# Performance work log

Measured on AMD Instinct MI355X. Metric: run time of the kernel, lower is better.

The kernel has to match this reference:

```python
import jax, jax.numpy as jnp
import numpy as np

KERNELS = (7, 9, 11)   # kernel_sizes, dilation=1 each
HEADS_PER = 2          # num_head // len(kernel_sizes)
HEAD_DIM = 32          # dim // num_head
DIM = 192


def _win_idx(L, K):
    # NATTEN non-causal window start: centered, clamped to stay in-bounds.
    starts = jnp.clip(jnp.arange(L) - K // 2, 0, L - K)
    return starts[:, None] + jnp.arange(K)[None, :]  # [L, K]


def _na2d(q, k, v, K):
    # q,k,v: [B, h, H, W, D]; q pre-scaled. Neighborhood attention, kernel KxK.
    B, h, H, W, D = q.shape
    ih = _win_idx(H, K)  # [H, K]
    iw = _win_idx(W, K)  # [W, K]
    kr = k[:, :, ih]     # [B, h, H, Kh, W, D]  rows gathered once
    # loop over the Kw kernel taps (small fixed structural loop)
    attn = jnp.stack(
        [jnp.einsum('bnijd,bnikjd->bnijk', q, kr[:, :, :, :, iw[:, kw], :])
         for kw in range(K)], axis=-1)                 # [B,h,H,W,Kh,Kw]
    attn = jax.nn.softmax(attn.reshape(B, h, H, W, K * K), axis=-1)
    attn = attn.reshape(B, h, H, W, K, K)
    vr = v[:, :, ih]     # [B, h, H, Kh, W, D]
    y = jnp.zeros_like(q)
    for kw in range(K):
        y = y + jnp.einsum('bnijk,bnikjd->bnijd',
                           attn[..., kw], vr[:, :, :, :, iw[:, kw], :])
    return y             # [B, h, H, W, D]


def _forward(x, w_qkv, b_qkv, w_proj, b_proj):
    B, H, W, C = x.shape
    qkv = x @ w_qkv + b_qkv                      # [B,H,W,3*DIM]
    scale = HEAD_DIM ** -0.5
    outs = []
    off = 0
    for K in KERNELS:
        ch = 3 * HEADS_PER * HEAD_DIM            # 192 per scale
        xi = qkv[..., off:off + ch]
        off += ch
        r = xi.reshape(B, H, W, 3, HEADS_PER, HEAD_DIM)
        q = jnp.transpose(r[:, :, :, 0], (0, 3, 1, 2, 4)) * scale
        k = jnp.transpose(r[:, :, :, 1], (0, 3, 1, 2, 4))
        v = jnp.transpose(r[:, :, :, 2], (0, 3, 1, 2, 4))
        y = _na2d(q, k, v, K)                    # [B,h,H,W,D]
        outs.append(jnp.transpose(y, (0, 2, 3, 1, 4)).reshape(B, H, W, HEADS_PER * HEAD_DIM))
    out = jnp.concatenate(outs, axis=-1)         # [B,H,W,DIM]
    return out @ w_proj + b_proj


def setup_inputs() -> dict:
    key = jax.random.key(0)
    ks = jax.random.split(key, 4)
    x = jax.random.normal(ks[0], (4, 96, 96, DIM), jnp.float32)
    w_qkv = jax.random.normal(ks[1], (DIM, 3 * DIM), jnp.float32) * 0.02
    b_qkv = jnp.zeros((3 * DIM,), jnp.float32)
    w_proj = jax.random.normal(ks[2], (DIM, DIM), jnp.float32) * 0.02
    b_proj = jnp.zeros((DIM,), jnp.float32)
    return {'x': x, 'w_qkv': w_qkv, 'b_qkv': b_qkv, 'w_proj': w_proj, 'b_proj': b_proj}


def reference(x, w_qkv, b_qkv, w_proj, b_proj):
    return _forward(x, w_qkv, b_qkv, w_proj, b_proj)
```

## Files before the change

### kernel.cpp

```cpp
#include <hip/hip_runtime.h>
#include <cstddef>

constexpr int B_ = 4, H_ = 96, W_ = 96, C_ = 192, QKVC = 576;
constexpr int NPIX = B_ * H_ * W_;
constexpr float SCALE = 0.17677669529663689f;

typedef __attribute__((ext_vector_type(8))) short bf16x8;
typedef __attribute__((ext_vector_type(4))) float f32x4;
typedef unsigned short ushort_t;

__device__ __forceinline__ unsigned short f2bf(float f) {
    unsigned int u = __builtin_bit_cast(unsigned int, f);
    u += 0x7fffu + ((u >> 16) & 1u);
    return (unsigned short)(u >> 16);
}
__device__ __forceinline__ float bf2f(unsigned short h) {
    unsigned int u = ((unsigned int)h) << 16;
    return __builtin_bit_cast(float, u);
}
__device__ __forceinline__ unsigned int pack2(unsigned short a, unsigned short b) {
    return (unsigned int)a | ((unsigned int)b << 16);
}

__global__ __launch_bounds__(256) void convert_x_kernel(
    const float* __restrict__ x, ushort_t* __restrict__ xh, int n4)
{
    int i = blockIdx.x * 256 + threadIdx.x;
    if (i >= n4) return;
    float4 v = ((const float4*)x)[i];
    uint2 p;
    p.x = pack2(f2bf(v.x), f2bf(v.y));
    p.y = pack2(f2bf(v.z), f2bf(v.w));
    ((uint2*)xh)[i] = p;
}

__global__ __launch_bounds__(256) void convert_w_kernel(
    const float* __restrict__ w_qkv, const float* __restrict__ w_proj,
    ushort_t* __restrict__ wqt, ushort_t* __restrict__ wpt_h,
    ushort_t* __restrict__ wpt_l)
{
    int idx = blockIdx.x * 256 + threadIdx.x;
    if (idx < 576 * 192) {
        int n = idx / 192, k = idx - n * 192;
        wqt[idx] = f2bf(w_qkv[(size_t)k * 576 + n]);
    } else {
        int i2 = idx - 576 * 192;
        if (i2 < 192 * 192) {
            int n = i2 / 192, k = i2 - n * 192;
            float v = w_proj[(size_t)k * 192 + n];
            unsigned short h = f2bf(v);
            wpt_h[i2] = h;
            wpt_l[i2] = f2bf(v - bf2f(h));
        }
    }
}

template<bool BSPLIT, bool OUTBF, bool VT>
__global__ __launch_bounds__(256) void gemm_mfma2_kernel(
    const ushort_t* __restrict__ A,
    const ushort_t* __restrict__ Bt_h, const ushort_t* __restrict__ Bt_l,
    const float* __restrict__ bias, void* __restrict__ Cout,
    ushort_t* __restrict__ vTout, int M, int N, int K)
{
    constexpr int NPB = BSPLIT ? 2 : 1;
    __shared__ __align__(16) ushort_t As[8 * 64 * 8];
    __shared__ __align__(16) ushort_t Bs[NPB][8 * 192 * 8];

    const int tid = threadIdx.x;
    const int lane = tid & 63;
    const int w = tid >> 6;
    const int wm = (w & 1) * 32;
    const int wn = (w >> 1) * 96;
    const int fm = lane & 15;
    const int fq = lane >> 4;

    const int ntiles = N / 192;
    const int m0 = (blockIdx.x / ntiles) * 64;
    const int n0 = (blockIdx.x % ntiles) * 192;

    f32x4 acc[2][6];
    #pragma unroll
    for (int mi = 0; mi < 2; ++mi)
        #pragma unroll
        for (int ni = 0; ni < 6; ++ni)
            acc[mi][ni] = (f32x4){0.f, 0.f, 0.f, 0.f};

    for (int k0 = 0; k0 < K; k0 += 64) {
        __syncthreads();
        #pragma unroll
        for (int it = 0; it < 2; ++it) {
            int idx = it * 256 + tid;
            int m = idx >> 3, kc = idx & 7;
            uint4 v = *(const uint4*)(A + (size_t)(m0 + m) * K + k0 + kc * 8);
            *(uint4*)(&As[0] + (kc * 64 + (m ^ kc)) * 8) = v;
        }
        #pragma unroll
        for (int it = 0; it < 6; ++it) {
            int idx = it * 256 + tid;
            int n = idx >> 3, kc = idx & 7;
            int phys = kc * 192 + (n ^ kc);
            *(uint4*)(&Bs[0][0] + phys * 8) =
                *(const uint4*)(Bt_h + (size_t)(n0 + n) * K + k0 + kc * 8);
            if constexpr (BSPLIT)
                *(uint4*)(&Bs[NPB - 1][0] + phys * 8) =
                    *(const uint4*)(Bt_l + (size_t)(n0 + n) * K + k0 + kc * 8);
        }
        __syncthreads();

        #pragma unroll
        for (int kt2 = 0; kt2 < 2; ++kt2) {
            const int kc = kt2 * 4 + fq;
            bf16x8 ah[2], bh[6];
            #pragma unroll
            for (int mi = 0; mi < 2; ++mi)
                ah[mi] = *(const bf16x8*)(&As[0] + (kc * 64 + ((wm + mi * 16 + fm) ^ kc)) * 8);
            #pragma unroll
            for (int ni = 0; ni < 6; ++ni)
                bh[ni] = *(const bf16x8*)(&Bs[0][0] + (kc * 192 + ((wn + ni * 16 + fm) ^ kc)) * 8);
            #pragma unroll
            for (int mi = 0; mi < 2; ++mi)
                #pragma unroll
                for (int ni = 0; ni < 6; ++ni)
                    acc[mi][ni] = __builtin_amdgcn_mfma_f32_16x16x32_bf16(
                        ah[mi], bh[ni], acc[mi][ni], 0, 0, 0);
            if constexpr (BSPLIT) {
                bf16x8 bl[6];
                #pragma unroll
                for (int ni = 0; ni < 6; ++ni)
                    bl[ni] = *(const bf16x8*)(&Bs[NPB - 1][0] + (kc * 192 + ((wn + ni * 16 + fm) ^ kc)) * 8);
                #pragma unroll
                for (int mi = 0; mi < 2; ++mi)
                    #pragma unroll
                    for (int ni = 0; ni < 6; ++ni)
                        acc[mi][ni] = __builtin_amdgcn_mfma_f32_16x16x32_bf16(
                            ah[mi], bl[ni], acc[mi][ni], 0, 0, 0);
            }
        }
    }

    #pragma unroll
    for (int ni = 0; ni < 6; ++ni) {
        const int lcol = wn + ni * 16 + fm;
        const int col = n0 + lcol;
        const float bv = bias[col];
        const int vl = lcol - 128;
        #pragma unroll
        for (int mi = 0; mi < 2; ++mi) {
            const int rbase = m0 + wm + mi * 16 + fq * 4;
            #pragma unroll
            for (int r = 0; r < 4; ++r) {
                float val = acc[mi][ni][r] + bv;
                if constexpr (OUTBF)
                    ((ushort_t*)Cout)[(size_t)(rbase + r) * N + col] = f2bf(val);
                else
                    ((float*)Cout)[(size_t)(rbase + r) * N + col] = val;
                if constexpr (VT) {
                    if (vl >= 0) {
                        int pix = rbase + r;
                        int bb = pix / 9216;
                        int rem = pix - bb * 9216;
                        int ii = rem / 96;
                        int jj = rem - ii * 96;
                        int hh = vl >> 5, dd = vl & 31;
                        vTout[((size_t)((bb * 96 + ii) * 6) + (n0 / 192) * 2 + hh) * 3072
                              + dd * 96 + jj] = f2bf(val);
                    }
                }
            }
        }
    }
}

__global__ __launch_bounds__(384, 5) void na2d_kernel(
    const ushort_t* __restrict__ qkv, const ushort_t* __restrict__ vT,
    ushort_t* __restrict__ attn)
{
    __shared__ ushort_t Kb[2][96 * 40];
    __shared__ ushort_t Vtb[2][32 * 104];
    __shared__ ushort_t Pb[6][16 * 40];

    int idx = blockIdx.x;
    const int g = idx % 3; idx /= 3;
    const int h = idx & 1; idx >>= 1;
    const int i = idx % 96;
    const int b = idx / 96;

    const int K = 7 + 2 * g, cc = K >> 1;
    int si = i - cc; if (si < 0) si = 0; if (si > H_ - K) si = H_ - K;

    const int tid = threadIdx.x;
    const int w = tid >> 6, lane = tid & 63;
    const int fm = lane & 15, fq = lane >> 4;
    const int pixbase = w * 16;

    int cb = (pixbase - cc) & ~7;
    if (cb < 0) cb = 0; if (cb > 64) cb = 64;
    const int col0 = cb + fm, col1 = cb + 16 + fm;

    int sj[4];
    #pragma unroll
    for (int r = 0; r < 4; ++r) {
        int jj = pixbase + fq * 4 + r - cc;
        if (jj < 0) jj = 0; if (jj > W_ - K) jj = W_ - K;
        sj[r] = jj;
    }

    const size_t rowstride = (size_t)W_ * QKVC;
    const bf16x8 qfrag = *(const bf16x8*)(
        qkv + (size_t)(b * H_ + i) * rowstride + (size_t)(pixbase + fm) * QKVC
        + g * 192 + h * 32 + fq * 8);

    const int scol = tid >> 2, sch = tid & 3;
    const size_t kgoff = (size_t)scol * QKVC + g * 192 + 64 + h * 32 + sch * 8;
    const int klds = scol * 40 + ((sch ^ (scol & 3)) << 3);
    const int vd = tid / 12, vc8 = tid - vd * 12;
    const int vlds = vd * 104 + vc8 * 8;
    const size_t vslice = ((size_t)((b * H_ + si) * 6) + g * 2 + h) * 3072;

    f32x4 y0 = {0.f, 0.f, 0.f, 0.f}, y1 = {0.f, 0.f, 0.f, 0.f};
    float lacc[4] = {0.f, 0.f, 0.f, 0.f};

    uint4 kv = *(const uint4*)(qkv + (size_t)(b * H_ + si) * rowstride + kgoff);
    uint4 vv = *(const uint4*)(vT + vslice + (size_t)tid * 8);

    for (int t = 0; t < K; ++t) {
        *(uint4*)&Kb[t & 1][klds] = kv;
        *(uint4*)&Vtb[t & 1][vlds] = vv;
        if (t + 1 < K) {
            kv = *(const uint4*)(qkv + (size_t)(b * H_ + si + t + 1) * rowstride + kgoff);
            vv = *(const uint4*)(vT + vslice + (size_t)(t + 1) * 18432 + (size_t)tid * 8);
        }
        __syncthreads();

        bf16x8 kf0 = *(const bf16x8*)&Kb[t & 1][col0 * 40 + ((fq ^ (col0 & 3)) << 3)];
        bf16x8 kf1 = *(const bf16x8*)&Kb[t & 1][col1 * 40 + ((fq ^ (col1 & 3)) << 3)];
        f32x4 s0 = __builtin_amdgcn_mfma_f32_16x16x32_bf16(
            qfrag, kf0, (f32x4){0.f, 0.f, 0.f, 0.f}, 0, 0, 0);
        f32x4 s1 = __builtin_amdgcn_mfma_f32_16x16x32_bf16(
            qfrag, kf1, (f32x4){0.f, 0.f, 0.f, 0.f}, 0, 0, 0);

        #pragma unroll
        for (int r = 0; r < 4; ++r) {
            float e0 = __expf(s0[r] * SCALE);
            float e1 = __expf(s1[r] * SCALE);
            e0 = ((unsigned)(col0 - sj[r]) < (unsigned)K) ? e0 : 0.f;
            e1 = ((unsigned)(col1 - sj[r]) < (unsigned)K) ? e1 : 0.f;
            unsigned short p0 = f2bf(e0), p1 = f2bf(e1);
            lacc[r] += bf2f(p0) + bf2f(p1);
            const int m = fq * 4 + r;
            Pb[w][m * 40 + (((fm >> 3) ^ (m & 3)) << 3) + (fm & 7)] = p0;
            Pb[w][m * 40 + ((((fm >> 3) + 2) ^ (m & 3)) << 3) + (fm & 7)] = p1;
        }

        bf16x8 pf = *(const bf16x8*)&Pb[w][fm * 40 + ((fq ^ (fm & 3)) << 3)];
        bf16x8 vf0 = *(const bf16x8*)&Vtb[t & 1][fm * 104 + cb + fq * 8];
        bf16x8 vf1 = *(const bf16x8*)&Vtb[t & 1][(16 + fm) * 104 + cb + fq * 8];
        y0 = __builtin_amdgcn_mfma_f32_16x16x32_bf16(pf, vf0, y0, 0, 0, 0);
        y1 = __builtin_amdgcn_mfma_f32_16x16x32_bf16(pf, vf1, y1, 0, 0, 0);
    }

    #pragma unroll
    for (int r = 0; r < 4; ++r) {
        float l = lacc[r];
        l += __shfl_xor(l, 1); l += __shfl_xor(l, 2);
        l += __shfl_xor(l, 4); l += __shfl_xor(l, 8);
        const float inv = 1.f / l;
        const int j = pixbase + fq * 4 + r;
        const size_t o = (size_t)((b * H_ + i) * W_ + j) * C_ + g * 64 + h * 32 + fm;
        attn[o]      = f2bf(y0[r] * inv);
        attn[o + 16] = f2bf(y1[r] * inv);
    }
}

extern "C" void kernel_launch(void* const* d_in, const int* in_sizes, int n_in,
                              void* d_out, int out_size, void* d_ws, size_t ws_size,
                              hipStream_t stream)
{
    const float* x      = (const float*)d_in[0];
    const float* w_qkv  = (const float*)d_in[1];
    const float* b_qkv  = (const float*)d_in[2];
    const float* w_proj = (const float*)d_in[3];
    const float* b_proj = (const float*)d_in[4];
    float* out = (float*)d_out;

    char* ws = (char*)d_ws;
    ushort_t* qkvh  = (ushort_t*)ws;
    char*     reg1  = ws + (size_t)NPIX * QKVC * 2;
    ushort_t* xh    = (ushort_t*)reg1;
    ushort_t* attn  = (ushort_t*)reg1;
    char*     wbase = reg1 + (size_t)NPIX * C_ * 2;
    ushort_t* wqt   = (ushort_t*)wbase;
    ushort_t* wpt_h = (ushort_t*)(wbase + 576 * 192 * 2);
    ushort_t* wpt_l = (ushort_t*)(wbase + 576 * 192 * 2 + 192 * 192 * 2);
    ushort_t* vT    = (ushort_t*)(wbase + 576 * 192 * 2 + 2 * 192 * 192 * 2);

    convert_x_kernel<<<(NPIX * C_ / 4 + 255) / 256, 256, 0, stream>>>(
        x, xh, NPIX * C_ / 4);
    convert_w_kernel<<<(576 * 192 + 192 * 192 + 255) / 256, 256, 0, stream>>>(
        w_qkv, w_proj, wqt, wpt_h, wpt_l);

    gemm_mfma2_kernel<false, true, true><<<(NPIX / 64) * (QKVC / 192), 256, 0, stream>>>(
        xh, wqt, nullptr, b_qkv, qkvh, vT, NPIX, QKVC, C_);

    na2d_kernel<<<2304, 384, 0, stream>>>(qkvh, vT, attn);

    gemm_mfma2_kernel<true, false, false><<<(NPIX / 64) * (C_ / 192), 256, 0, stream>>>(
        attn, wpt_h, wpt_l, b_proj, out, nullptr, NPIX, C_, C_);
}
```

Measured before the change: 187.8 us.

## Load NA2D K/V fragments directly from global, drop shared staging and barriers

The neighborhood-attention kernel stops staging K and V^T rows through double-buffered shared memory with a block barrier each tap. Each lane now loads its MFMA fragments straight from global memory, prefetched one tap ahead in registers. The kernel also remaps block IDs so consecutive physical blocks are spread across XCD-style groups of 8, and lowers the occupancy hint from 5 to 4. Separately, the QKV GEMM no longer writes V columns to the row-major output, since they already go to the transposed buffer. The trade-off is redundant global and L2 traffic across overlapping waves and more register pressure, in exchange for removing LDS traffic and synchronisation.

```diff
diff --git a/kernel.cpp b/kernel.cpp
--- a/kernel.cpp
+++ b/kernel.cpp
@@ -150,10 +150,7 @@
             #pragma unroll
             for (int r = 0; r < 4; ++r) {
                 float val = acc[mi][ni][r] + bv;
-                if constexpr (OUTBF)
-                    ((ushort_t*)Cout)[(size_t)(rbase + r) * N + col] = f2bf(val);
-                else
-                    ((float*)Cout)[(size_t)(rbase + r) * N + col] = val;
+                bool skipc = false;
                 if constexpr (VT) {
                     if (vl >= 0) {
                         int pix = rbase + r;
@@ -164,22 +161,29 @@
                         int hh = vl >> 5, dd = vl & 31;
                         vTout[((size_t)((bb * 96 + ii) * 6) + (n0 / 192) * 2 + hh) * 3072
                               + dd * 96 + jj] = f2bf(val);
+                        skipc = true;
                     }
                 }
+                if (!skipc) {
+                    if constexpr (OUTBF)
+                        ((ushort_t*)Cout)[(size_t)(rbase + r) * N + col] = f2bf(val);
+                    else
+                        ((float*)Cout)[(size_t)(rbase + r) * N + col] = val;
+                }
             }
         }
     }
 }
 
-__global__ __launch_bounds__(384, 5) void na2d_kernel(
+__global__ __launch_bounds__(384, 4) void na2d_kernel(
     const ushort_t* __restrict__ qkv, const ushort_t* __restrict__ vT,
     ushort_t* __restrict__ attn)
 {
-    __shared__ ushort_t Kb[2][96 * 40];
-    __shared__ ushort_t Vtb[2][32 * 104];
     __shared__ ushort_t Pb[6][16 * 40];
 
-    int idx = blockIdx.x;
+    int phys = blockIdx.x;
+    int idx = (phys & 7) * 288 + (phys >> 3);
+
     const int g = idx % 3; idx /= 3;
     const int h = idx & 1; idx >>= 1;
     const int i = idx % 96;
@@ -210,34 +214,36 @@
         qkv + (size_t)(b * H_ + i) * rowstride + (size_t)(pixbase + fm) * QKVC
         + g * 192 + h * 32 + fq * 8);
 
-    const int scol = tid >> 2, sch = tid & 3;
-    const size_t kgoff = (size_t)scol * QKVC + g * 192 + 64 + h * 32 + sch * 8;
-    const int klds = scol * 40 + ((sch ^ (scol & 3)) << 3);
-    const int vd = tid / 12, vc8 = tid - vd * 12;
-    const int vlds = vd * 104 + vc8 * 8;
+    const ushort_t* kp0 = qkv + (size_t)(b * H_ + si) * rowstride
+        + (size_t)col0 * QKVC + g * 192 + 64 + h * 32 + fq * 8;
+    const ushort_t* kp1 = kp0 + (size_t)16 * QKVC;
     const size_t vslice = ((size_t)((b * H_ + si) * 6) + g * 2 + h) * 3072;
+    const ushort_t* vp0 = vT + vslice + (size_t)fm * 96 + cb + fq * 8;
+    const ushort_t* vp1 = vp0 + 16 * 96;
 
     f32x4 y0 = {0.f, 0.f, 0.f, 0.f}, y1 = {0.f, 0.f, 0.f, 0.f};
     float lacc[4] = {0.f, 0.f, 0.f, 0.f};
 
-    uint4 kv = *(const uint4*)(qkv + (size_t)(b * H_ + si) * rowstride + kgoff);
-    uint4 vv = *(const uint4*)(vT + vslice + (size_t)tid * 8);
+    bf16x8 kf0 = *(const bf16x8*)kp0;
+    bf16x8 kf1 = *(const bf16x8*)kp1;
+    bf16x8 vf0 = *(const bf16x8*)vp0;
+    bf16x8 vf1 = *(const bf16x8*)vp1;
 
     for (int t = 0; t < K; ++t) {
-        *(uint4*)&Kb[t & 1][klds] = kv;
-        *(uint4*)&Vtb[t & 1][vlds] = vv;
+        const bf16x8 ck0 = kf0, ck1 = kf1, cv0 = vf0, cv1 = vf1;
         if (t + 1 < K) {
-            kv = *(const uint4*)(qkv + (size_t)(b * H_ + si + t + 1) * rowstride + kgoff);
-            vv = *(const uint4*)(vT + vslice + (size_t)(t + 1) * 18432 + (size_t)tid * 8);
-        }
-        __syncthreads();
-
-        bf16x8 kf0 = *(const bf16x8*)&Kb[t & 1][col0 * 40 + ((fq ^ (col0 & 3)) << 3)];
-        bf16x8 kf1 = *(const bf16x8*)&Kb[t & 1][col1 * 40 + ((fq ^ (col1 & 3)) << 3)];
+            kp0 += rowstride; kp1 += rowstride;
+            vp0 += 18432;     vp1 += 18432;
+            kf0 = *(const bf16x8*)kp0;
+            kf1 = *(const bf16x8*)kp1;
+            vf0 = *(const bf16x8*)vp0;
+            vf1 = *(const bf16x8*)vp1;
+        }
+
         f32x4 s0 = __builtin_amdgcn_mfma_f32_16x16x32_bf16(
-            qfrag, kf0, (f32x4){0.f, 0.f, 0.f, 0.f}, 0, 0, 0);
+            qfrag, ck0, (f32x4){0.f, 0.f, 0.f, 0.f}, 0, 0, 0);
         f32x4 s1 = __builtin_amdgcn_mfma_f32_16x16x32_bf16(
-            qfrag, kf1, (f32x4){0.f, 0.f, 0.f, 0.f}, 0, 0, 0);
+            qfrag, ck1, (f32x4){0.f, 0.f, 0.f, 0.f}, 0, 0, 0);
 
         #pragma unroll
         for (int r = 0; r < 4; ++r) {
@@ -253,10 +259,8 @@
         }
 
         bf16x8 pf = *(const bf16x8*)&Pb[w][fm * 40 + ((fq ^ (fm & 3)) << 3)];
-        bf16x8 vf0 = *(const bf16x8*)&Vtb[t & 1][fm * 104 + cb + fq * 8];
-        bf16x8 vf1 = *(const bf16x8*)&Vtb[t & 1][(16 + fm) * 104 + cb + fq * 8];
-        y0 = __builtin_amdgcn_mfma_f32_16x16x32_bf16(pf, vf0, y0, 0, 0, 0);
-        y1 = __builtin_amdgcn_mfma_f32_16x16x32_bf16(pf, vf1, y1, 0, 0, 0);
+        y0 = __builtin_amdgcn_mfma_f32_16x16x32_bf16(pf, cv0, y0, 0, 0, 0);
+        y1 = __builtin_amdgcn_mfma_f32_16x16x32_bf16(pf, cv1, y1, 0, 0, 0);
     }
 
     #pragma unroll
```

After: 186.0 us. No clear change (-0.9%).
